# Kernel tuning notes

Measured on AMD Instinct MI355X. Metric: run time of the kernel, lower is better.

Reference implementation:

```python
import jax, jax.numpy as jnp
import numpy as np

N = 8192        # nodes
E = 131072      # template edges (avg degree 16)
IN_DIM = 2
H = 128         # hidden_dim
Z = 128         # z_dim
MAX_DEPTH = 32
DEPTH_PERTURB = 2
NEG = -1e30


def setup_inputs() -> dict:
    key = jax.random.key(0)
    ks = jax.random.split(key, 24)
    s = 0.05
    # template node features: col0 = node type in {0,1,2}, col1 = placeholder
    types = jax.random.randint(ks[0], (N,), 0, 3)
    x = jnp.stack([types.astype(jnp.float32),
                   jax.random.normal(ks[1], (N,))], axis=1)
    edge_index = jax.random.randint(ks[2], (2, E), 0, N)
    node_depth = jnp.sort(jax.random.randint(ks[3], (N,), 0, MAX_DEPTH))
    z = jax.random.normal(ks[4], (Z,))
    return {
        "x": x, "z": z,
        "edge_index": edge_index, "node_depth": node_depth,
        # GCNConv 1 & 2 (PyG style: y = x @ W^T, symmetric-normalized agg, + bias)
        "conv1_w": jax.random.normal(ks[5], (H, IN_DIM)) * s,
        "conv1_b": jnp.zeros((H,)),
        "conv2_w": jax.random.normal(ks[6], (H, H)) * s,
        "conv2_b": jnp.zeros((H,)),
        # node_proj: Linear(H+Z,H) -> ReLU -> Linear(H,H)
        "np1_w": jax.random.normal(ks[7], (H, H + Z)) * s,
        "np1_b": jnp.zeros((H,)),
        "np2_w": jax.random.normal(ks[8], (H, H)) * s,
        "np2_b": jnp.zeros((H,)),
        # src/tgt projections (bias-free)
        "src_w": jax.random.normal(ks[9], (H, H)) * s,
        "tgt_w": jax.random.normal(ks[10], (H, H)) * s,
        # inv_mlp: Linear(2H+Z,H) -> ReLU -> Linear(H,1)
        "inv1_w": jax.random.normal(ks[11], (H, 2 * H + Z)) * s,
        "inv1_b": jnp.zeros((H,)),
        "inv2_w": jax.random.normal(ks[12], (1, H)) * s,
        "inv2_b": jnp.zeros((1,)),
    }


def _gcn_conv(x, src, dst, W, b, n):
    # PyG GCNConv with self loops: out_i = sum_j norm_ij * (x_j W^T) + b
    xw = x @ W.T                                             # [n, out]
    deg = jax.ops.segment_sum(jnp.ones(src.shape, xw.dtype), dst,
                              num_segments=n) + 1.0          # self-loop
    rsq = jax.lax.rsqrt(deg)
    msg = (rsq[src] * rsq[dst])[:, None] * xw[src]           # [E, out]
    agg = jax.ops.segment_sum(msg, dst, num_segments=n)
    agg = agg + xw / deg[:, None]                            # self-loop term
    return agg + b


def reference(x, z, edge_index, node_depth,
              conv1_w, conv1_b, conv2_w, conv2_b,
              np1_w, np1_b, np2_w, np2_b,
              src_w, tgt_w, inv1_w, inv1_b, inv2_w, inv2_b):
    n = x.shape[0]
    types = x[:, 0].astype(jnp.int32)
    src, dst = edge_index[0], edge_index[1]

    # --- GCN encode ---
    h = jax.nn.relu(_gcn_conv(x, src, dst, conv1_w, conv1_b, n))
    h = jax.nn.relu(_gcn_conv(h, src, dst, conv2_w, conv2_b, n))

    # --- node_proj with broadcast z ---
    hz = jnp.concatenate([h, jnp.broadcast_to(z[None, :], (n, Z))], axis=1)
    h = jax.nn.relu(hz @ np1_w.T + np1_b) @ np2_w.T + np2_b  # [n, H]

    # --- vectorized per-target candidate attention scores ---
    Ht = h @ tgt_w.T                                         # [n, H]
    Hs = h @ src_w.T                                         # [n, H]
    scores = Ht @ Hs.T                                       # [n, n]: S[v,u]
    depth = node_depth
    # candidate u valid for target v iff depth[u] <= depth[v]-1+perturb
    cand_mask = depth[None, :] <= (depth[:, None] - 1 + DEPTH_PERTURB)
    scores_m = jnp.where(cand_mask, scores, NEG)
    top_vals, top_idx = jax.lax.top_k(scores_m, 2)           # [n,2] each

    num_cand = cand_mask.sum(axis=1)
    target_valid = (depth >= 1) & (types != 0)
    # type==2 (AND) gets k=2 fanins, other non-PI types k=1
    valid = jnp.stack([target_valid & (num_cand >= 1),
                       target_valid & (types == 2) & (num_cand >= 2)], axis=1)

    # --- per-edge inversion-bit MLP (vectorized over [n, 2] chosen edges) ---
    h_u = h[top_idx]                                         # [n,2,H]
    h_v = jnp.broadcast_to(h[:, None, :], (n, 2, H))
    z_b = jnp.broadcast_to(z[None, None, :], (n, 2, Z))
    inv_in = jnp.concatenate([h_u, h_v, z_b], axis=-1)       # [n,2,2H+Z]
    inv_logit = (jax.nn.relu(inv_in @ inv1_w.T + inv1_b) @ inv2_w.T + inv2_b)[..., 0]
    inv_bit = (jax.nn.sigmoid(inv_logit) > 0.5).astype(jnp.int32)

    return top_vals, inv_logit, top_idx, inv_bit, valid
```

## Files before the change

### kernel.cpp

```cpp
#include <hip/hip_runtime.h>

#define NN 8192
#define EE 131072
#define HH 128
#define NEGV -1.0e30f
#define SEG 128
#define NSEG (NN / SEG)
#define VT 128

typedef __attribute__((ext_vector_type(8))) short bf16x8;
typedef __attribute__((ext_vector_type(4))) float f32x4;

__device__ __forceinline__ unsigned short f2bf(float f) {
    unsigned int u = __float_as_uint(f);
    unsigned int r = u + 0x7fffu + ((u >> 16) & 1u);
    return (unsigned short)(r >> 16);
}
__device__ __forceinline__ float bf2f(unsigned short b) {
    return __uint_as_float((unsigned int)b << 16);
}


__global__ __launch_bounds__(256) void k_deg(const int* __restrict__ dst, int* __restrict__ degi) {
    int t = blockIdx.x * 256 + threadIdx.x;
    if (t < EE) atomicAdd(&degi[dst[t]], 1);
}

__global__ __launch_bounds__(1024) void k_scan(const int* __restrict__ degi, int* __restrict__ rowptr,
                                               float* __restrict__ dinv, float* __restrict__ rsq) {
    __shared__ int ls[1024];
    int tid = threadIdx.x;
    int base = tid * 8;
    int loc[8]; int s = 0;
#pragma unroll
    for (int i = 0; i < 8; i++) {
        int dg = degi[base + i];
        loc[i] = s; s += dg;
        double d = (double)(dg + 1);
        dinv[base + i] = (float)(1.0 / d);
        rsq[base + i] = (float)(1.0 / sqrt(d));
    }
    ls[tid] = s; __syncthreads();
    int tot = s;
    for (int d = 1; d < 1024; d <<= 1) {
        int v = (tid >= d) ? ls[tid - d] : 0;
        __syncthreads();
        ls[tid] += v;
        __syncthreads();
    }
    int pre = ls[tid] - tot;
#pragma unroll
    for (int i = 0; i < 8; i++) rowptr[base + i] = pre + loc[i];
    if (tid == 1023) rowptr[NN] = pre + tot;
}

__global__ __launch_bounds__(256) void k_fill(const int* __restrict__ src, const int* __restrict__ dst,
                                              const int* __restrict__ rowptr, int* __restrict__ cursor,
                                              int* __restrict__ ecsr) {
    int t = blockIdx.x * 256 + threadIdx.x;
    if (t < EE) {
        int d = dst[t];
        int pos = atomicAdd(&cursor[d], 1);
        ecsr[rowptr[d] + pos] = src[t];
    }
}


__global__ __launch_bounds__(256) void k_gather1(const int* __restrict__ rowptr, const int* __restrict__ ecsr,
                                                 const float* __restrict__ rsq, const float* __restrict__ dinv,
                                                 const float* __restrict__ x, const float* __restrict__ w,
                                                 const float* __restrict__ bias, float* __restrict__ out) {
    int g = blockIdx.x * 256 + threadIdx.x;
    int d = g >> 6, lane = g & 63;
    if (d >= NN) return;
    float w0a = w[lane * 2], w1a = w[lane * 2 + 1];
    float w0b = w[(lane + 64) * 2], w1b = w[(lane + 64) * 2 + 1];
    int s0 = rowptr[d], s1 = rowptr[d + 1];
    float rd = rsq[d];
    float a0 = 0.f, a1 = 0.f;
    for (int sl = s0; sl < s1; sl++) {
        int s = ecsr[sl];
        float x0 = x[s * 2], x1 = x[s * 2 + 1];
        float f = rsq[s] * rd;
        a0 = fmaf(f, x0 * w0a + x1 * w1a, a0);
        a1 = fmaf(f, x0 * w0b + x1 * w1b, a1);
    }
    float x0d = x[d * 2], x1d = x[d * 2 + 1], di = dinv[d];
    a0 = fmaf(x0d * w0a + x1d * w1a, di, a0) + bias[lane];
    a1 = fmaf(x0d * w0b + x1d * w1b, di, a1) + bias[64 + lane];
    out[d * HH + lane] = fmaxf(a0, 0.f);
    out[d * HH + 64 + lane] = fmaxf(a1, 0.f);
}


__global__ __launch_bounds__(256) void k_gather2(const int* __restrict__ rowptr, const int* __restrict__ ecsr,
                                                 const float* __restrict__ rsq, const float* __restrict__ dinv,
                                                 const float* __restrict__ xw, const float* __restrict__ bias,
                                                 float* __restrict__ out) {
    int g = blockIdx.x * 256 + threadIdx.x;
    int d = g >> 6, lane = g & 63;
    if (d >= NN) return;
    int s0 = rowptr[d], s1 = rowptr[d + 1];
    float rd = rsq[d];
    float a0 = 0.f, a1 = 0.f;
    for (int sl = s0; sl < s1; sl++) {
        int s = ecsr[sl];
        float f = rsq[s] * rd;
        a0 = fmaf(f, xw[s * HH + lane], a0);
        a1 = fmaf(f, xw[s * HH + 64 + lane], a1);
    }
    float di = dinv[d];
    a0 = fmaf(xw[d * HH + lane], di, a0) + bias[lane];
    a1 = fmaf(xw[d * HH + 64 + lane], di, a1) + bias[64 + lane];
    out[d * HH + lane] = fmaxf(a0, 0.f);
    out[d * HH + 64 + lane] = fmaxf(a1, 0.f);
}


__global__ __launch_bounds__(256) void k_prep(const float* __restrict__ conv2_w, const float* __restrict__ np1_w,
                                              const float* __restrict__ np2_w, const float* __restrict__ src_w,
                                              const float* __restrict__ tgt_w, const float* __restrict__ inv1_w,
                                              const float* __restrict__ np1_b, const float* __restrict__ inv1_b,
                                              const float* __restrict__ z, float* __restrict__ T,
                                              float* __restrict__ c1, float* __restrict__ cz) {
    int y = blockIdx.y;
    if (y < 7) {
        int t = blockIdx.x * 256 + threadIdx.x;
        int j = t >> 7, k = t & 127;
        const float* W; int stride, off;
        switch (y) {
            case 0:  W = conv2_w; stride = 128; off = 0;   break;
            case 1:  W = np1_w;   stride = 256; off = 0;   break;
            case 2:  W = np2_w;   stride = 128; off = 0;   break;
            case 3:  W = src_w;   stride = 128; off = 0;   break;
            case 4:  W = tgt_w;   stride = 128; off = 0;   break;
            case 5:  W = inv1_w;  stride = 384; off = 0;   break;
            default: W = inv1_w;  stride = 384; off = 128; break;
        }
        T[y * 16384 + k * 128 + j] = W[j * stride + off + k];
    } else if (blockIdx.x == 0) {
        int tid = threadIdx.x;
        if (tid < 128) {
            float s = np1_b[tid];
            for (int k = 0; k < 128; k++) s += z[k] * np1_w[tid * 256 + 128 + k];
            c1[tid] = s;
        } else {
            int j = tid - 128;
            float s = inv1_b[j];
            for (int k = 0; k < 128; k++) s += z[k] * inv1_w[j * 384 + 256 + k];
            cz[j] = s;
        }
    }
}


__global__ __launch_bounds__(256) void k_gemm128(const float* __restrict__ A, const float* __restrict__ WT,
                                                 const float* __restrict__ bias, float* __restrict__ out,
                                                 int relu) {
    __shared__ float As[32][33];
    __shared__ float Bs[32][128];
    int tid = threadIdx.x;
    int tx = tid & 31, ty = tid >> 5;
    int row0 = blockIdx.x * 32;
    float acc[4][4] = {};
    for (int k0 = 0; k0 < 128; k0 += 32) {
        {
            int r = tid >> 3, k = (tid & 7) << 2;
            float4 v = *(const float4*)&A[(row0 + r) * HH + k0 + k];
            As[r][k] = v.x; As[r][k + 1] = v.y; As[r][k + 2] = v.z; As[r][k + 3] = v.w;
        }
#pragma unroll
        for (int i = 0; i < 4; i++) {
            int kk = (tid >> 5) + i * 8;
            int c = (tid & 31) << 2;
            *(float4*)&Bs[kk][c] = *(const float4*)&WT[(k0 + kk) * HH + c];
        }
        __syncthreads();
#pragma unroll 8
        for (int kk = 0; kk < 32; kk++) {
            float a0 = As[ty * 4 + 0][kk], a1 = As[ty * 4 + 1][kk];
            float a2 = As[ty * 4 + 2][kk], a3 = As[ty * 4 + 3][kk];
            float4 b = *(const float4*)&Bs[kk][tx * 4];
            acc[0][0] = fmaf(a0, b.x, acc[0][0]); acc[0][1] = fmaf(a0, b.y, acc[0][1]);
            acc[0][2] = fmaf(a0, b.z, acc[0][2]); acc[0][3] = fmaf(a0, b.w, acc[0][3]);
            acc[1][0] = fmaf(a1, b.x, acc[1][0]); acc[1][1] = fmaf(a1, b.y, acc[1][1]);
            acc[1][2] = fmaf(a1, b.z, acc[1][2]); acc[1][3] = fmaf(a1, b.w, acc[1][3]);
            acc[2][0] = fmaf(a2, b.x, acc[2][0]); acc[2][1] = fmaf(a2, b.y, acc[2][1]);
            acc[2][2] = fmaf(a2, b.z, acc[2][2]); acc[2][3] = fmaf(a2, b.w, acc[2][3]);
            acc[3][0] = fmaf(a3, b.x, acc[3][0]); acc[3][1] = fmaf(a3, b.y, acc[3][1]);
            acc[3][2] = fmaf(a3, b.z, acc[3][2]); acc[3][3] = fmaf(a3, b.w, acc[3][3]);
        }
        __syncthreads();
    }
#pragma unroll
    for (int i = 0; i < 4; i++) {
        float4 v = make_float4(acc[i][0], acc[i][1], acc[i][2], acc[i][3]);
        if (bias) {
            v.x += bias[tx * 4]; v.y += bias[tx * 4 + 1];
            v.z += bias[tx * 4 + 2]; v.w += bias[tx * 4 + 3];
        }
        if (relu) {
            v.x = fmaxf(v.x, 0.f); v.y = fmaxf(v.y, 0.f);
            v.z = fmaxf(v.z, 0.f); v.w = fmaxf(v.w, 0.f);
        }
        *(float4*)&out[(row0 + ty * 4 + i) * HH + tx * 4] = v;
    }
}


__global__ __launch_bounds__(256) void k_mlp(const float* __restrict__ h2g, const float* __restrict__ T,
                                             const float* __restrict__ c1, const float* __restrict__ np2_b,
                                             float* __restrict__ h3g,
                                             unsigned short* __restrict__ HtP, unsigned short* __restrict__ HsP) {
    __shared__ float bufA[32][132];
    __shared__ float bufB[32][132];
    __shared__ float Bs[32][128];
    int tid = threadIdx.x;
    int tx = tid & 31, ty = tid >> 5;
    int row0 = blockIdx.x * 32;
#pragma unroll
    for (int p = 0; p < 4; p++) {
        int q = p * 256 + tid;
        int r = q >> 5, c4 = (q & 31) * 4;
        *(float4*)&bufA[r][c4] = *(const float4*)&h2g[(size_t)(row0 + r) * HH + c4];
    }
    __syncthreads();
    for (int g = 0; g < 4; g++) {
        const float* WT;
        switch (g) {
            case 0:  WT = T + 1 * 16384; break;
            case 1:  WT = T + 2 * 16384; break;
            case 2:  WT = T + 4 * 16384; break;
            default: WT = T + 3 * 16384; break;
        }
        float (*src)[132] = (g == 1) ? bufB : bufA;
        float acc[4][4] = {};
        for (int k0 = 0; k0 < 128; k0 += 32) {
#pragma unroll
            for (int i = 0; i < 4; i++) {
                int kk = (tid >> 5) + i * 8;
                int c = (tid & 31) << 2;
                *(float4*)&Bs[kk][c] = *(const float4*)&WT[(k0 + kk) * HH + c];
            }
            __syncthreads();
#pragma unroll 8
            for (int kk = 0; kk < 32; kk++) {
                float a0 = src[ty * 4 + 0][k0 + kk], a1 = src[ty * 4 + 1][k0 + kk];
                float a2 = src[ty * 4 + 2][k0 + kk], a3 = src[ty * 4 + 3][k0 + kk];
                float4 b = *(const float4*)&Bs[kk][tx * 4];
                acc[0][0] = fmaf(a0, b.x, acc[0][0]); acc[0][1] = fmaf(a0, b.y, acc[0][1]);
                acc[0][2] = fmaf(a0, b.z, acc[0][2]); acc[0][3] = fmaf(a0, b.w, acc[0][3]);
                acc[1][0] = fmaf(a1, b.x, acc[1][0]); acc[1][1] = fmaf(a1, b.y, acc[1][1]);
                acc[1][2] = fmaf(a1, b.z, acc[1][2]); acc[1][3] = fmaf(a1, b.w, acc[1][3]);
                acc[2][0] = fmaf(a2, b.x, acc[2][0]); acc[2][1] = fmaf(a2, b.y, acc[2][1]);
                acc[2][2] = fmaf(a2, b.z, acc[2][2]); acc[2][3] = fmaf(a2, b.w, acc[2][3]);
                acc[3][0] = fmaf(a3, b.x, acc[3][0]); acc[3][1] = fmaf(a3, b.y, acc[3][1]);
                acc[3][2] = fmaf(a3, b.z, acc[3][2]); acc[3][3] = fmaf(a3, b.w, acc[3][3]);
            }
            __syncthreads();
        }
        if (g == 0) {
#pragma unroll
            for (int i = 0; i < 4; i++)
#pragma unroll
                for (int jj = 0; jj < 4; jj++)
                    bufB[ty * 4 + i][tx * 4 + jj] = fmaxf(acc[i][jj] + c1[tx * 4 + jj], 0.f);
        } else if (g == 1) {
#pragma unroll
            for (int i = 0; i < 4; i++) {
                float4 v;
                v.x = acc[i][0] + np2_b[tx * 4 + 0];
                v.y = acc[i][1] + np2_b[tx * 4 + 1];
                v.z = acc[i][2] + np2_b[tx * 4 + 2];
                v.w = acc[i][3] + np2_b[tx * 4 + 3];
                bufA[ty * 4 + i][tx * 4 + 0] = v.x; bufA[ty * 4 + i][tx * 4 + 1] = v.y;
                bufA[ty * 4 + i][tx * 4 + 2] = v.z; bufA[ty * 4 + i][tx * 4 + 3] = v.w;
                *(float4*)&h3g[(size_t)(row0 + ty * 4 + i) * HH + tx * 4] = v;
            }
        } else {
            unsigned short* PP = (g == 2) ? HtP : HsP;
            int chunk = tx >> 3;
            int cic = (tx * 4) & 31;
#pragma unroll
            for (int i = 0; i < 4; i++) {
                int row = row0 + ty * 4 + i;
                size_t off = (size_t)row * 384 + chunk * 96 + cic;
                unsigned short h[4], m[4], lo[4];
#pragma unroll
                for (int jj = 0; jj < 4; jj++) {
                    float val = acc[i][jj];
                    unsigned short hb = f2bf(val);
                    float r1 = val - bf2f(hb);
                    unsigned short mb = f2bf(r1);
                    float r2 = r1 - bf2f(mb);
                    h[jj] = hb; m[jj] = mb; lo[jj] = f2bf(r2);
                }
                *(uint2*)&PP[off] = make_uint2((unsigned)h[0] | ((unsigned)h[1] << 16),
                                               (unsigned)h[2] | ((unsigned)h[3] << 16));
                *(uint2*)&PP[off + 32] = make_uint2((unsigned)m[0] | ((unsigned)m[1] << 16),
                                                    (unsigned)m[2] | ((unsigned)m[3] << 16));
                *(uint2*)&PP[off + 64] = make_uint2((unsigned)lo[0] | ((unsigned)lo[1] << 16),
                                                    (unsigned)lo[2] | ((unsigned)lo[3] << 16));
            }
        }
    }
}


__global__ __launch_bounds__(256) void k_cnt_valid(const int* __restrict__ depth, const float* __restrict__ x,
                                                   int* __restrict__ cnt, float* __restrict__ out) {
    int v = blockIdx.x * 256 + threadIdx.x;
    if (v >= NN) return;
    int limit = depth[v] + 1;
    int lo = 0, hi = NN;
    while (lo < hi) { int mid = (lo + hi) >> 1; if (depth[mid] <= limit) lo = mid + 1; else hi = mid; }
    cnt[v] = lo;
    int type = (int)(x[v * 2] + 0.5f);
    bool tv = (depth[v] >= 1) && (type != 0);
    out[4 * NN * 2 + v * 2 + 0] = (tv && lo >= 1) ? 1.0f : 0.0f;
    out[4 * NN * 2 + v * 2 + 1] = (tv && type == 2 && lo >= 2) ? 1.0f : 0.0f;
}


__global__ __launch_bounds__(64) void k_tiles(const int* __restrict__ cnt, int* __restrict__ nact,
                                              int* __restrict__ tlist, int* __restrict__ ntiles) {
    int lane = threadIdx.x;
    int cmax = cnt[lane * VT + VT - 1];
    int n = (cmax + SEG - 1) / SEG;
    nact[lane] = n;
    int x = n;
    for (int off = 1; off < 64; off <<= 1) {
        int y = __shfl_up(x, off, 64);
        if (lane >= off) x += y;
    }
    int base = x - n;
    for (int s = 0; s < n; s++) tlist[base + s] = (lane << 8) | s;
    if (lane == 63) *ntiles = x;
}


__global__ __launch_bounds__(256, 2) void k_top2_stage1(
    const unsigned short* __restrict__ HtP, const unsigned short* __restrict__ HsP,
    const int* __restrict__ cnt, const int* __restrict__ tlist,
    const int* __restrict__ ntiles, int* __restrict__ tctr,
    float* __restrict__ pval, int* __restrict__ pidx) {
    __shared__ unsigned short Bsh[64 * 392];
    __shared__ int tsh;
    int tid = threadIdx.x;
    int wave = tid >> 6, lane = tid & 63;
    int l = lane & 15, quad = lane >> 4;
    int nt = *ntiles;
    for (;;) {
        __syncthreads();
        if (tid == 0) tsh = atomicAdd(tctr, 1);
        __syncthreads();
        int t = tsh;
        if (t >= nt) return;
        int code = tlist[t];
        int v0 = (code >> 8) * VT;
        int seg = code & 255;
        int ub0 = seg * SEG;
        int vbase = v0 + wave * 32;
        bf16x8 afr[2][4][3];
#pragma unroll
        for (int s = 0; s < 2; s++) {
            const unsigned short* ap = &HtP[(size_t)(vbase + s * 16 + l) * 384 + quad * 8];
#pragma unroll
            for (int c = 0; c < 4; c++) {
                afr[s][c][0] = *(const bf16x8*)&ap[c * 96];
                afr[s][c][1] = *(const bf16x8*)&ap[c * 96 + 32];
                afr[s][c][2] = *(const bf16x8*)&ap[c * 96 + 64];
            }
        }
        int creg[8];
#pragma unroll
        for (int i = 0; i < 8; i++)
            creg[i] = cnt[vbase + (i >> 2) * 16 + quad * 4 + (i & 3)];
        float t1v[8], t2v[8]; int t1i[8], t2i[8];
#pragma unroll
        for (int i = 0; i < 8; i++) { t1v[i] = NEGV; t2v[i] = NEGV; t1i[i] = 0x7fffffff; t2i[i] = 0x7fffffff; }
        int cmax = cnt[v0 + VT - 1];
        int uend = ub0 + SEG; if (uend > cmax) uend = cmax;
        for (int cb = ub0; cb < uend; cb += 64) {
            __syncthreads();
#pragma unroll
            for (int gi = 0; gi < 12; gi++) {
                int g = gi * 256 + tid;
                int r = g / 48, w = g - r * 48;
                *(uint4*)&Bsh[r * 392 + w * 8] = *(const uint4*)&HsP[(size_t)(cb + r) * 384 + w * 8];
            }
            __syncthreads();
            int cend = cb + 64; if (cend > uend) cend = uend;
            for (int u0 = cb; u0 < cend; u0 += 16) {
                int u = u0 + l;
                const unsigned short* bp = &Bsh[(u0 - cb + l) * 392 + quad * 8];
                f32x4 acc0 = {0.f, 0.f, 0.f, 0.f}, acc1 = {0.f, 0.f, 0.f, 0.f};
#pragma unroll
                for (int c = 0; c < 4; c++) {
                    bf16x8 bh = *(const bf16x8*)&bp[c * 96];
                    bf16x8 bm = *(const bf16x8*)&bp[c * 96 + 32];
                    bf16x8 bl = *(const bf16x8*)&bp[c * 96 + 64];
                    acc0 = __builtin_amdgcn_mfma_f32_16x16x32_bf16(afr[0][c][0], bh, acc0, 0, 0, 0);
                    acc1 = __builtin_amdgcn_mfma_f32_16x16x32_bf16(afr[1][c][0], bh, acc1, 0, 0, 0);
                    acc0 = __builtin_amdgcn_mfma_f32_16x16x32_bf16(afr[0][c][0], bm, acc0, 0, 0, 0);
                    acc1 = __builtin_amdgcn_mfma_f32_16x16x32_bf16(afr[1][c][0], bm, acc1, 0, 0, 0);
                    acc0 = __builtin_amdgcn_mfma_f32_16x16x32_bf16(afr[0][c][1], bh, acc0, 0, 0, 0);
                    acc1 = __builtin_amdgcn_mfma_f32_16x16x32_bf16(afr[1][c][1], bh, acc1, 0, 0, 0);
                    acc0 = __builtin_amdgcn_mfma_f32_16x16x32_bf16(afr[0][c][0], bl, acc0, 0, 0, 0);
                    acc1 = __builtin_amdgcn_mfma_f32_16x16x32_bf16(afr[1][c][0], bl, acc1, 0, 0, 0);
                    acc0 = __builtin_amdgcn_mfma_f32_16x16x32_bf16(afr[0][c][2], bh, acc0, 0, 0, 0);
                    acc1 = __builtin_amdgcn_mfma_f32_16x16x32_bf16(afr[1][c][2], bh, acc1, 0, 0, 0);
                    acc0 = __builtin_amdgcn_mfma_f32_16x16x32_bf16(afr[0][c][1], bm, acc0, 0, 0, 0);
                    acc1 = __builtin_amdgcn_mfma_f32_16x16x32_bf16(afr[1][c][1], bm, acc1, 0, 0, 0);
                }
#pragma unroll
                for (int i = 0; i < 8; i++) {
                    float sv = (i < 4) ? acc0[i & 3] : acc1[i & 3];
                    float val = (u < creg[i]) ? sv : NEGV;
                    if (val > t1v[i] || (val == t1v[i] && u < t1i[i])) {
                        t2v[i] = t1v[i]; t2i[i] = t1i[i]; t1v[i] = val; t1i[i] = u;
                    } else if (val > t2v[i] || (val == t2v[i] && u < t2i[i])) {
                        t2v[i] = val; t2i[i] = u;
                    }
                }
            }
        }
#pragma unroll
        for (int m = 1; m <= 8; m <<= 1) {
#pragma unroll
            for (int i = 0; i < 8; i++) {
                float ov1 = __shfl_xor(t1v[i], m, 64);
                int   oi1 = __shfl_xor(t1i[i], m, 64);
                float ov2 = __shfl_xor(t2v[i], m, 64);
                int   oi2 = __shfl_xor(t2i[i], m, 64);
                bool b1 = (ov1 > t1v[i]) || (ov1 == t1v[i] && oi1 < t1i[i]);
                float w1v = b1 ? ov1 : t1v[i]; int w1i = b1 ? oi1 : t1i[i];
                float l1v = b1 ? t1v[i] : ov1; int l1i = b1 ? t1i[i] : oi1;
                float c2v = b1 ? ov2 : t2v[i]; int c2i = b1 ? oi2 : t2i[i];
                bool b2 = (l1v > c2v) || (l1v == c2v && l1i < c2i);
                t1v[i] = w1v; t1i[i] = w1i;
                t2v[i] = b2 ? l1v : c2v; t2i[i] = b2 ? l1i : c2i;
            }
        }
        if (l == 0) {
#pragma unroll
            for (int i = 0; i < 8; i++) {
                int v = vbase + (i >> 2) * 16 + quad * 4 + (i & 3);
                int o = (v * NSEG + seg) * 2;
                pval[o] = t1v[i];     pidx[o] = t1i[i];
                pval[o + 1] = t2v[i]; pidx[o + 1] = t2i[i];
            }
        }
    }
}


__global__ __launch_bounds__(256) void k_merge_inv(const float* __restrict__ pval, const int* __restrict__ pidx,
                                                   const int* __restrict__ nact,
                                                   const float* __restrict__ P, const float* __restrict__ Q,
                                                   const float* __restrict__ cz, const float* __restrict__ w2,
                                                   const float* __restrict__ b2, float* __restrict__ out) {
    int gid = blockIdx.x * 256 + threadIdx.x;
    int v = gid >> 6, lane = gid & 63;
    if (v >= NN) return;
    int na = nact[v >> 7];
    float v1 = NEGV, v2 = NEGV; int i1 = 0x7fffffff, i2 = 0x7fffffff;
    if (lane < na) {
        int o = (v * NSEG + lane) * 2;
        v1 = pval[o];     i1 = pidx[o];
        v2 = pval[o + 1]; i2 = pidx[o + 1];
    }
#pragma unroll
    for (int m = 1; m <= 32; m <<= 1) {
        float ov1 = __shfl_xor(v1, m, 64);
        int   oi1 = __shfl_xor(i1, m, 64);
        float ov2 = __shfl_xor(v2, m, 64);
        int   oi2 = __shfl_xor(i2, m, 64);
        bool b1 = (ov1 > v1) || (ov1 == v1 && oi1 < i1);
        float w1v = b1 ? ov1 : v1; int w1i = b1 ? oi1 : i1;
        float l1v = b1 ? v1 : ov1; int l1i = b1 ? i1 : oi1;
        float c2v = b1 ? ov2 : v2; int c2i = b1 ? oi2 : i2;
        bool b2 = (l1v > c2v) || (l1v == c2v && l1i < c2i);
        v1 = w1v; i1 = w1i;
        v2 = b2 ? l1v : c2v; i2 = b2 ? l1i : c2i;
    }
    if (na == 0) { v1 = NEGV; v2 = NEGV; i1 = 0; i2 = 1; }
    int u1 = i1, u2 = i2;
    float cza = cz[lane], czb = cz[64 + lane];
    float w2a = w2[lane], w2b = w2[64 + lane];
    float Qa = Q[(size_t)v * HH + lane], Qb = Q[(size_t)v * HH + 64 + lane];
    float p0 = fmaxf(P[(size_t)u1 * HH + lane] + Qa + cza, 0.f) * w2a +
               fmaxf(P[(size_t)u1 * HH + 64 + lane] + Qb + czb, 0.f) * w2b;
    float p1 = fmaxf(P[(size_t)u2 * HH + lane] + Qa + cza, 0.f) * w2a +
               fmaxf(P[(size_t)u2 * HH + 64 + lane] + Qb + czb, 0.f) * w2b;
#pragma unroll
    for (int off = 32; off >= 1; off >>= 1) {
        p0 += __shfl_down(p0, off, 64);
        p1 += __shfl_down(p1, off, 64);
    }
    if (lane == 0) {
        float bb = b2[0];
        float l0 = p0 + bb, l1 = p1 + bb;
        out[v * 2 + 0] = v1; out[v * 2 + 1] = v2;
        out[NN * 2 + v * 2 + 0] = l0;
        out[NN * 2 + v * 2 + 1] = l1;
        out[2 * NN * 2 + v * 2 + 0] = (float)i1;
        out[2 * NN * 2 + v * 2 + 1] = (float)i2;
        out[3 * NN * 2 + v * 2 + 0] = (l0 > 0.f) ? 1.f : 0.f;
        out[3 * NN * 2 + v * 2 + 1] = (l1 > 0.f) ? 1.f : 0.f;
    }
}


extern "C" void kernel_launch(void* const* d_in, const int* in_sizes, int n_in,
                              void* d_out, int out_size, void* d_ws, size_t ws_size,
                              hipStream_t stream) {
    const float* x       = (const float*)d_in[0];
    const float* z       = (const float*)d_in[1];
    const int*   eidx    = (const int*)d_in[2];
    const int*   depth   = (const int*)d_in[3];
    const float* conv1_w = (const float*)d_in[4];
    const float* conv1_b = (const float*)d_in[5];
    const float* conv2_w = (const float*)d_in[6];
    const float* conv2_b = (const float*)d_in[7];
    const float* np1_w   = (const float*)d_in[8];
    const float* np1_b   = (const float*)d_in[9];
    const float* np2_w   = (const float*)d_in[10];
    const float* np2_b   = (const float*)d_in[11];
    const float* src_w   = (const float*)d_in[12];
    const float* tgt_w   = (const float*)d_in[13];
    const float* inv1_w  = (const float*)d_in[14];
    const float* inv1_b  = (const float*)d_in[15];
    const float* inv2_w  = (const float*)d_in[16];
    const float* inv2_b  = (const float*)d_in[17];
    float* out = (float*)d_out;
    float* wsf = (float*)d_ws;

    const int NH = NN * HH;
    float* R0 = wsf;
    float* R1 = wsf + (size_t)NH;
    unsigned short* HtP = (unsigned short*)R1;
    unsigned short* HsP = HtP + 3 * (size_t)NH;
    float* P = wsf + (size_t)NH;
    float* Q = wsf + 2 * (size_t)NH;
    float* pval = wsf + 4 * (size_t)NH;
    int*   pidx = (int*)(wsf + 5 * (size_t)NH);
    float* T  = wsf + 6 * (size_t)NH;
    float* c1 = T + 7 * 16384;
    float* cz = c1 + 128;
    float* rsq  = cz + 128;
    float* dinv = rsq + NN;
    int* degi   = (int*)(dinv + NN);
    int* rowptr = degi + NN;
    int* cursor = rowptr + NN + 1;
    int* cnt    = cursor + NN;
    int* nact   = cnt + NN;
    int* ntiles = nact + 64;
    int* tctr   = ntiles + 1;
    int* tlist  = tctr + 1;
    int* ecsr   = tlist + 4096;

    const int* esrc = eidx;
    const int* edst = eidx + EE;

    hipMemsetAsync(degi, 0, NN * sizeof(int), stream);
    hipMemsetAsync(cursor, 0, NN * sizeof(int), stream);
    hipMemsetAsync(tctr, 0, sizeof(int), stream);
    k_prep<<<dim3(64, 8), 256, 0, stream>>>(conv2_w, np1_w, np2_w, src_w, tgt_w, inv1_w,
                                            np1_b, inv1_b, z, T, c1, cz);
    k_deg<<<EE / 256, 256, 0, stream>>>(edst, degi);
    k_scan<<<1, 1024, 0, stream>>>(degi, rowptr, dinv, rsq);
    k_fill<<<EE / 256, 256, 0, stream>>>(esrc, edst, rowptr, cursor, ecsr);
    k_gather1<<<NN * 64 / 256, 256, 0, stream>>>(rowptr, ecsr, rsq, dinv, x, conv1_w, conv1_b, R0);
    k_gemm128<<<256, 256, 0, stream>>>(R0, T + 0 * 16384, nullptr, R1, 0);
    k_gather2<<<NN * 64 / 256, 256, 0, stream>>>(rowptr, ecsr, rsq, dinv, R1, conv2_b, R0);
    k_mlp<<<256, 256, 0, stream>>>(R0, T, c1, np2_b, R0, HtP, HsP);
    k_cnt_valid<<<NN / 256, 256, 0, stream>>>(depth, x, cnt, out);
    k_tiles<<<1, 64, 0, stream>>>(cnt, nact, tlist, ntiles);
    k_top2_stage1<<<768, 256, 0, stream>>>(HtP, HsP, cnt, tlist, ntiles, tctr, pval, pidx);
    k_gemm128<<<256, 256, 0, stream>>>(R0, T + 5 * 16384, nullptr, P, 0);
    k_gemm128<<<256, 256, 0, stream>>>(R0, T + 6 * 16384, nullptr, Q, 0);
    k_merge_inv<<<NN / 4, 256, 0, stream>>>(pval, pidx, nact, P, Q, cz, inv2_w, inv2_b, out);
}
```

Measured before the change: 336.3 us.

## Double-buffer B tiles via direct global-to-LDS loads and simplify top-2 update

```diff
diff --git a/kernel.cpp b/kernel.cpp
--- a/kernel.cpp
+++ b/kernel.cpp
@@ -10,6 +10,9 @@
 
 typedef __attribute__((ext_vector_type(8))) short bf16x8;
 typedef __attribute__((ext_vector_type(4))) float f32x4;
+
+typedef __attribute__((address_space(1))) unsigned int AS1U;
+typedef __attribute__((address_space(3))) unsigned int AS3U;
 
 __device__ __forceinline__ unsigned short f2bf(float f) {
     unsigned int u = __float_as_uint(f);
@@ -339,12 +342,25 @@
 }
 
 
+__device__ __forceinline__ void stage32(unsigned short* buf, const unsigned short* __restrict__ HsP,
+                                        int cb, int wave, int lane) {
+    if (lane < 48) {
+        const unsigned short* g0 = HsP + (size_t)(cb + wave * 8) * 384 + lane * 8;
+        unsigned short* l0 = buf + wave * 8 * 392;
+#pragma unroll
+        for (int k = 0; k < 8; k++) {
+            __builtin_amdgcn_global_load_lds((const AS1U*)(g0 + (size_t)k * 384),
+                                             (AS3U*)(l0 + k * 392), 16, 0, 0);
+        }
+    }
+}
+
 __global__ __launch_bounds__(256, 2) void k_top2_stage1(
     const unsigned short* __restrict__ HtP, const unsigned short* __restrict__ HsP,
     const int* __restrict__ cnt, const int* __restrict__ tlist,
     const int* __restrict__ ntiles, int* __restrict__ tctr,
     float* __restrict__ pval, int* __restrict__ pidx) {
-    __shared__ unsigned short Bsh[64 * 392];
+    __shared__ unsigned short Bsh[2][32 * 392];
     __shared__ int tsh;
     int tid = threadIdx.x;
     int wave = tid >> 6, lane = tid & 63;
@@ -361,6 +377,10 @@
         int seg = code & 255;
         int ub0 = seg * SEG;
         int vbase = v0 + wave * 32;
+        int cmax = cnt[v0 + VT - 1];
+        int uend = ub0 + SEG; if (uend > cmax) uend = cmax;
+        int nch = (uend - ub0 + 31) >> 5;
+        stage32(Bsh[0], HsP, ub0, wave, lane);
         bf16x8 afr[2][4][3];
 #pragma unroll
         for (int s = 0; s < 2; s++) {
@@ -379,21 +399,15 @@
         float t1v[8], t2v[8]; int t1i[8], t2i[8];
 #pragma unroll
         for (int i = 0; i < 8; i++) { t1v[i] = NEGV; t2v[i] = NEGV; t1i[i] = 0x7fffffff; t2i[i] = 0x7fffffff; }
-        int cmax = cnt[v0 + VT - 1];
-        int uend = ub0 + SEG; if (uend > cmax) uend = cmax;
-        for (int cb = ub0; cb < uend; cb += 64) {
-            __syncthreads();
-#pragma unroll
-            for (int gi = 0; gi < 12; gi++) {
-                int g = gi * 256 + tid;
-                int r = g / 48, w = g - r * 48;
-                *(uint4*)&Bsh[r * 392 + w * 8] = *(const uint4*)&HsP[(size_t)(cb + r) * 384 + w * 8];
-            }
-            __syncthreads();
-            int cend = cb + 64; if (cend > uend) cend = uend;
+        __syncthreads();
+        for (int ci = 0; ci < nch; ci++) {
+            int cb = ub0 + ci * 32;
+            if (ci + 1 < nch) stage32(Bsh[(ci + 1) & 1], HsP, cb + 32, wave, lane);
+            const unsigned short* bbase = Bsh[ci & 1];
+            int cend = cb + 32; if (cend > uend) cend = uend;
             for (int u0 = cb; u0 < cend; u0 += 16) {
                 int u = u0 + l;
-                const unsigned short* bp = &Bsh[(u0 - cb + l) * 392 + quad * 8];
+                const unsigned short* bp = &bbase[(u0 - cb + l) * 392 + quad * 8];
                 f32x4 acc0 = {0.f, 0.f, 0.f, 0.f}, acc1 = {0.f, 0.f, 0.f, 0.f};
 #pragma unroll
                 for (int c = 0; c < 4; c++) {
@@ -416,14 +430,16 @@
 #pragma unroll
                 for (int i = 0; i < 8; i++) {
                     float sv = (i < 4) ? acc0[i & 3] : acc1[i & 3];
-                    float val = (u < creg[i]) ? sv : NEGV;
-                    if (val > t1v[i] || (val == t1v[i] && u < t1i[i])) {
-                        t2v[i] = t1v[i]; t2i[i] = t1i[i]; t1v[i] = val; t1i[i] = u;
-                    } else if (val > t2v[i] || (val == t2v[i] && u < t2i[i])) {
-                        t2v[i] = val; t2i[i] = u;
-                    }
+                    bool gt1 = (u < creg[i]) & (sv > t1v[i]);
+                    bool gt2 = (u < creg[i]) & (sv > t2v[i]);
+                    float n2v = gt1 ? t1v[i] : (gt2 ? sv : t2v[i]);
+                    int   n2i = gt1 ? t1i[i] : (gt2 ? u  : t2i[i]);
+                    t1v[i] = gt1 ? sv : t1v[i];
+                    t1i[i] = gt1 ? u  : t1i[i];
+                    t2v[i] = n2v; t2i[i] = n2i;
                 }
             }
+            __syncthreads();
         }
 #pragma unroll
         for (int m = 1; m <= 8; m <<= 1) {
@@ -484,7 +500,8 @@
         v1 = w1v; i1 = w1i;
         v2 = b2 ? l1v : c2v; i2 = b2 ? l1i : c2i;
     }
-    if (na == 0) { v1 = NEGV; v2 = NEGV; i1 = 0; i2 = 1; }
+    if (v1 == NEGV) { v2 = NEGV; i1 = 0; i2 = 1; }
+    else if (v2 == NEGV) { i2 = (i1 == 0) ? 1 : 0; }
     int u1 = i1, u2 = i2;
     float cza = cz[lane], czb = cz[64 + lane];
     float w2a = w2[lane], w2b = w2[64 + lane];
```

New measurement: 322.4 us. 1.04x faster.
